# Performance work log

Hardware: AMD Instinct MI355X
Metric: run time of the kernel (lower is better)

## Reference

```python
import jax, jax.numpy as jnp
import numpy as np
from jax import lax

B, Q, C, K = 256, 900, 91, 300  # batch, queries, classes, topk boxes for eval
SIGMA = 0.5                      # gaussian decay variance
SCORE_THR = 1e-3                 # hardcoded score_threshold in soft_nms


def setup_inputs() -> dict:
    key = jax.random.key(0)
    k1, k2, k3 = jax.random.split(key, 3)
    pred_logits = jax.random.normal(k1, (B, Q, C), dtype=jnp.float32)
    pred_boxes = jax.random.uniform(k2, (B, Q, 4), dtype=jnp.float32)  # cxcywh in [0,1]
    target_sizes = jax.random.randint(k3, (B, 2), 480, 1334).astype(jnp.float32)  # (h, w)
    return {"pred_logits": pred_logits, "pred_boxes": pred_boxes, "target_sizes": target_sizes}


def _iou_one(box, boxes):
    # box: [4] xyxy, boxes: [K,4] xyxy -> iou: [K]
    area1 = (box[2] - box[0]) * (box[3] - box[1])
    area2 = (boxes[:, 2] - boxes[:, 0]) * (boxes[:, 3] - boxes[:, 1])
    lt = jnp.maximum(box[:2], boxes[:, :2])
    rb = jnp.minimum(box[2:], boxes[:, 2:])
    wh = jnp.clip(rb - lt, 0.0)
    inter = wh[:, 0] * wh[:, 1]
    return inter / (area1 + area2 - inter)


def _soft_nms(boxes, scores):
    # boxes: [K,4], scores: [K]. Sequential gaussian soft-NMS, faithful to source
    # (source's iou_threshold arg is unused; decay applied to all trailing boxes).
    idxs = jnp.arange(K)

    def step(carry, i):
        bxs, scs, active = carry
        m = jnp.argmax(jnp.where(idxs >= i, scs, -jnp.inf))
        cond = active & (scs[m] >= SCORE_THR)  # break condition (sticky)
        # swap rows i <-> m
        bi, bm = bxs[i], bxs[m]
        si, sm = scs[i], scs[m]
        b2 = bxs.at[i].set(bm).at[m].set(bi)
        s2 = scs.at[i].set(sm).at[m].set(si)
        # gaussian decay on boxes after i
        decay = jnp.exp(-(_iou_one(b2[i], b2) ** 2) / SIGMA)
        s2 = s2 * jnp.where(idxs > i, decay, 1.0)
        return (jnp.where(cond, b2, bxs), jnp.where(cond, s2, scs), cond), None

    (boxes, scores, _), _ = lax.scan(step, (boxes, scores, jnp.array(True)), idxs)
    keep = scores > SCORE_THR
    return boxes, scores, keep


def _postprocess(pred_logits, pred_boxes, target_sizes):
    prob = jax.nn.sigmoid(pred_logits)                       # [B,Q,C]
    flat = prob.reshape(B, Q * C)
    topk_values, topk_indexes = lax.top_k(flat, K)           # [B,K]
    scores = topk_values
    topk_boxes = topk_indexes // C                           # query index
    labels = topk_indexes % C                                # class index
    # cxcywh -> xyxy
    cx, cy, w, h = jnp.split(pred_boxes, 4, axis=-1)
    xyxy = jnp.concatenate([cx - 0.5 * w, cy - 0.5 * h, cx + 0.5 * w, cy + 0.5 * h], axis=-1)
    gidx = jnp.broadcast_to(topk_boxes[..., None], (B, K, 4))
    boxes = jnp.take_along_axis(xyxy, gidx, axis=1)          # [B,K,4]
    img_h, img_w = target_sizes[:, 0], target_sizes[:, 1]
    scale = jnp.stack([img_w, img_h, img_w, img_h], axis=1)[:, None, :]
    boxes = boxes * scale
    boxes, scores, keep = jax.vmap(_soft_nms)(boxes, scores)
    return scores, labels, boxes, keep


def reference(pred_logits, pred_boxes, target_sizes):
    # Returns dense arrays + keep mask (ragged filtering expressed as a boolean mask
    # to stay jit-compatible). labels are intentionally NOT reordered by soft-NMS
    # swaps, matching the source's in-place mutation semantics.
    return _postprocess(pred_logits, pred_boxes, target_sizes)
```

## Files before the change

kernel.cpp:

```cpp
#include <hip/hip_runtime.h>
#include <cfloat>
#include <cmath>

#pragma clang fp contract(off)

#define BB 256
#define QQ 900
#define CC 91
#define KK 300
#define QC 81900
#define MAXIDX 81899
#define NF4 20475
#define STRIPC 30
#define SKCAP 512

#define OFF_SCORES 0
#define OFF_LABELS 76800
#define OFF_BOXES  153600
#define OFF_KEEP   460800

__device__ __forceinline__ unsigned int wave_max_u32(unsigned int x) {
#define DPP_MAX(ctrl, rmask)                                                   \
  { unsigned int tmp = (unsigned int)__builtin_amdgcn_update_dpp(              \
        (int)x, (int)x, ctrl, rmask, 0xF, false);                              \
    x = tmp > x ? tmp : x; }
  DPP_MAX(0x111, 0xF)
  DPP_MAX(0x112, 0xF)
  DPP_MAX(0x114, 0xF)
  DPP_MAX(0x118, 0xF)
  DPP_MAX(0x142, 0xA)
  DPP_MAX(0x143, 0xC)
#undef DPP_MAX
  return (unsigned int)__builtin_amdgcn_readlane((int)x, 63);
}

__device__ __forceinline__ float rdlane_f(float x, int l) {
  return __uint_as_float(
      (unsigned int)__builtin_amdgcn_readlane((int)__float_as_uint(x), l));
}

__device__ __forceinline__ float soft_decay(float s, float4 bb, float4 bm,
                                            float area1) {
  float area2 = (bb.z - bb.x) * (bb.w - bb.y);
  float ltx = fmaxf(bm.x, bb.x);
  float lty = fmaxf(bm.y, bb.y);
  float rbx = fminf(bm.z, bb.z);
  float rby = fminf(bm.w, bb.w);
  float whx = fmaxf(rbx - ltx, 0.0f);
  float why = fmaxf(rby - lty, 0.0f);
  float inter = whx * why;
  float iou = inter / ((area1 + area2) - inter);
  return s * expf(-(iou * iou) * 2.0f);
}

__global__ __launch_bounds__(256, 1) void fused_kernel(
    const float* __restrict__ logits,
    const float* __restrict__ boxes_in,
    const float* __restrict__ tsizes,
    float* __restrict__ out)
{
  const int b = blockIdx.x;
  const int t = threadIdx.x;
  const int lane = t & 63;
  const int w = t >> 6;

  __shared__ unsigned int strip[STRIPC + 1][256];
  __shared__ int hist[2048];
  __shared__ int suffix[256];
  __shared__ unsigned long long skey[SKCAP];
  __shared__ float  sc_lds[KK];
  __shared__ float4 bx_lds[KK];
  __shared__ unsigned long long wkey[2][4];
  __shared__ float4 wbox[2][4];
  __shared__ float  isc_s[2];
  __shared__ float4 ibx_s[2];
  __shared__ int cnt2, cstar_s, cutbin;

  if (t == 0) { cnt2 = 0; cstar_s = 0; cutbin = 0; }
  for (int i = t; i < 2048; i += 256) hist[i] = 0;
  __syncthreads();

  const float4* row = (const float4*)(logits + (size_t)b * QC);
  unsigned int nh = 0;

  float4 f[8];
#define PROC_ELEM(xv, idxv)                                                    \
  {                                                                            \
    bool hit = (xv) > 2.0f;                                                    \
    unsigned int pos = hit ? nh : (unsigned int)STRIPC;                        \
    strip[pos][t] = (unsigned int)(idxv);                                      \
    nh = hit ? nh + 1u : nh;                                                   \
    nh = nh > (unsigned int)STRIPC ? (unsigned int)STRIPC : nh;                \
  }

  for (int k0 = 0; k0 + 8 <= 79; k0 += 8) {
#pragma unroll
    for (int u = 0; u < 8; ++u) f[u] = row[t + (k0 + u) * 256];
#pragma unroll
    for (int u = 0; u < 8; ++u) {
      const int i4 = (t + (k0 + u) * 256) * 4;
      PROC_ELEM(f[u].x, i4 + 0)
      PROC_ELEM(f[u].y, i4 + 1)
      PROC_ELEM(f[u].z, i4 + 2)
      PROC_ELEM(f[u].w, i4 + 3)
    }
  }
  for (int k = 72; k < 79; ++k) {
    float4 x4 = row[t + k * 256];
    const int i4 = (t + k * 256) * 4;
    PROC_ELEM(x4.x, i4 + 0)
    PROC_ELEM(x4.y, i4 + 1)
    PROC_ELEM(x4.z, i4 + 2)
    PROC_ELEM(x4.w, i4 + 3)
  }
  if (t < NF4 - 79 * 256) {
    float4 x4 = row[t + 79 * 256];
    const int i4 = (t + 79 * 256) * 4;
    PROC_ELEM(x4.x, i4 + 0)
    PROC_ELEM(x4.y, i4 + 1)
    PROC_ELEM(x4.z, i4 + 2)
    PROC_ELEM(x4.w, i4 + 3)
  }
#undef PROC_ELEM

  const float* lrow = logits + (size_t)b * QC;
  for (unsigned int j = 0; j < nh; ++j) {
    unsigned int idx = strip[j][t];
    float x = lrow[idx];
    unsigned int bin = (__float_as_uint(x) - 0x40000000u) >> 13;
    bin = bin > 2047u ? 2047u : bin;
    atomicAdd(&hist[bin], 1);
  }
  __syncthreads();

  {
    int cs = 0;
#pragma unroll
    for (int k = 0; k < 8; ++k) cs += hist[t * 8 + k];
    suffix[t] = cs;
  }
  __syncthreads();
  for (int off = 1; off < 256; off <<= 1) {
    int add = (t + off < 256) ? suffix[t + off] : 0;
    __syncthreads();
    suffix[t] += add;
    __syncthreads();
  }
  if (suffix[t] >= KK && (t == 255 || suffix[t + 1] < KK)) cstar_s = t;
  __syncthreads();
  if (t == 0) {
    int cs = cstar_s;
    int acc = (cs < 255) ? suffix[cs + 1] : 0;
    for (int k = 7; k >= 0; --k) {
      acc += hist[cs * 8 + k];
      if (acc >= KK) { cutbin = cs * 8 + k; break; }
    }
  }
  __syncthreads();
  const int cb = cutbin;

  for (unsigned int j = 0; j < nh; ++j) {
    unsigned int idx = strip[j][t];
    float x = lrow[idx];
    unsigned int bin = (__float_as_uint(x) - 0x40000000u) >> 13;
    bin = bin > 2047u ? 2047u : bin;
    if ((int)bin >= cb) {
      float sgm = 1.0f / (1.0f + expf(-x));
      int p = atomicAdd(&cnt2, 1);
      if (p < SKCAP)
        skey[p] = ((unsigned long long)__float_as_uint(sgm) << 17) |
                  (unsigned long long)(MAXIDX - idx);
    }
  }
  __syncthreads();
  const int M = min(cnt2, SKCAP);

  const float img_h = tsizes[b * 2 + 0];
  const float img_w = tsizes[b * 2 + 1];
  for (int o = t; o < M; o += 256) {
    unsigned long long ko = skey[o];
    int r = 0;
    for (int k = 0; k < M; ++k) r += (skey[k] > ko) ? 1 : 0;
    if (r < KK) {
      unsigned int bits = (unsigned int)(ko >> 17);
      int idx = MAXIDX - (int)(ko & 0x1FFFFull);
      int q   = idx / CC;
      int lab = idx - q * CC;

      out[OFF_LABELS + b * KK + r] = (float)lab;
      sc_lds[r] = __uint_as_float(bits);

      float4 bxv = ((const float4*)boxes_in)[(size_t)b * QQ + q];
      float cx = bxv.x, cy = bxv.y, ww = bxv.z, hh = bxv.w;
      float4 bo;
      bo.x = (cx - 0.5f * ww) * img_w;
      bo.y = (cy - 0.5f * hh) * img_h;
      bo.z = (cx + 0.5f * ww) * img_w;
      bo.w = (cy + 0.5f * hh) * img_h;
      bx_lds[r] = bo;
    }
  }
  __syncthreads();

  const int e1 = t;
  const bool v2 = (lane < 11);
  const int e2 = 256 + w * 11 + lane;

  float  sc1 = sc_lds[e1];
  float4 bx1 = bx_lds[e1];
  float  sc2 = 0.0f;
  float4 bx2 = make_float4(0.f, 0.f, 0.f, 0.f);
  if (v2) { sc2 = sc_lds[e2]; bx2 = bx_lds[e2]; }

  for (int i = 0; i < KK; ++i) {
    const int p = i & 1;

    bool a1 = (e1 >= i);
    bool a2 = v2 && (e2 >= i);
    unsigned int u1 = a1 ? __float_as_uint(sc1) : 0u;
    unsigned int u2 = a2 ? __float_as_uint(sc2) : 0u;
    unsigned int um = u1 > u2 ? u1 : u2;
    unsigned int wm = wave_max_u32(um);
    unsigned long long m1 = __ballot(a1 && u1 == wm);
    unsigned long long m2 = __ballot(a2 && u2 == wm);
    int lstar;
    bool prim;
    if (m1) { lstar = __ffsll((long long)m1) - 1; prim = true; }
    else    { lstar = m2 ? __ffsll((long long)m2) - 1 : 0; prim = false; }
    int estar = prim ? (w * 64 + lstar) : (256 + w * 11 + lstar);
    float cbx, cby, cbz, cbw;
    if (prim) {
      cbx = rdlane_f(bx1.x, lstar); cby = rdlane_f(bx1.y, lstar);
      cbz = rdlane_f(bx1.z, lstar); cbw = rdlane_f(bx1.w, lstar);
    } else {
      cbx = rdlane_f(bx2.x, lstar); cby = rdlane_f(bx2.y, lstar);
      cbz = rdlane_f(bx2.z, lstar); cbw = rdlane_f(bx2.w, lstar);
    }
    if (lane == 0) {
      wkey[p][w] = ((unsigned long long)wm << 32) |
                   (unsigned long long)(511 - estar);
      wbox[p][w] = make_float4(cbx, cby, cbz, cbw);
    }
    if (e1 == i)        { isc_s[p] = sc1; ibx_s[p] = bx1; }
    if (v2 && e2 == i)  { isc_s[p] = sc2; ibx_s[p] = bx2; }
    __syncthreads();

    unsigned long long k0 = wkey[p][0], k1 = wkey[p][1], k2 = wkey[p][2],
                       k3 = wkey[p][3];
    float4 wb0 = wbox[p][0], wb1 = wbox[p][1], wb2 = wbox[p][2],
           wb3 = wbox[p][3];
    float  si = isc_s[p];
    float4 bi = ibx_s[p];

    unsigned long long best = k0;
    best = k1 > best ? k1 : best;
    best = k2 > best ? k2 : best;
    best = k3 > best ? k3 : best;
    float sm = __uint_as_float((unsigned int)(best >> 32));
    if (!(sm >= 0.001f)) break;
    int mi = 511 - (int)(best & 0x1FFull);
    int widx = (mi < 256) ? (mi >> 6) : ((mi - 256) / 11);
    float4 bm = wb0;
    if (widx == 1) bm = wb1;
    if (widx == 2) bm = wb2;
    if (widx == 3) bm = wb3;

    if (e1 == i)  { sc1 = sm; bx1 = bm; }
    if (e1 == mi) { sc1 = si; bx1 = bi; }
    if (v2) {
      if (e2 == i)  { sc2 = sm; bx2 = bm; }
      if (e2 == mi) { sc2 = si; bx2 = bi; }
    }

    float area1 = (bm.z - bm.x) * (bm.w - bm.y);
    if (e1 > i)       sc1 = soft_decay(sc1, bx1, bm, area1);
    if (v2 && e2 > i) sc2 = soft_decay(sc2, bx2, bm, area1);
  }

  out[OFF_SCORES + b * KK + e1] = sc1;
  ((float4*)(out + OFF_BOXES))[b * KK + e1] = bx1;
  out[OFF_KEEP + b * KK + e1] = (sc1 > 0.001f) ? 1.0f : 0.0f;
  if (v2) {
    out[OFF_SCORES + b * KK + e2] = sc2;
    ((float4*)(out + OFF_BOXES))[b * KK + e2] = bx2;
    out[OFF_KEEP + b * KK + e2] = (sc2 > 0.001f) ? 1.0f : 0.0f;
  }
}

extern "C" void kernel_launch(void* const* d_in, const int* in_sizes, int n_in,
                              void* d_out, int out_size, void* d_ws, size_t ws_size,
                              hipStream_t stream) {
  const float* pred_logits = (const float*)d_in[0];
  const float* pred_boxes  = (const float*)d_in[1];
  const float* tsizes      = (const float*)d_in[2];
  float* out = (float*)d_out;
  (void)d_ws; (void)ws_size;

  fused_kernel<<<BB, 256, 0, stream>>>(pred_logits, pred_boxes, tsizes, out);
}
```

Before: 349.2 us.

## Run soft-NMS loop in a single wavefront to drop per-iteration block barriers

The sequential soft-NMS loop moves from all four waves, which synchronised through LDS and __syncthreads every iteration, to wave 0 alone. Each lane holds five elements in registers, and the argmax, swap and decay use DPP reductions, ballots and readlane only. Box areas are cached per element so they are not recomputed each step. This removes 300 block barriers and LDS round trips per image, at the cost of each lane doing about five times more decay math per step, with the outer loop over the five register slots fully unrolled.

```diff
diff --git a/kernel.cpp b/kernel.cpp
--- a/kernel.cpp
+++ b/kernel.cpp
@@ -39,20 +39,6 @@
       (unsigned int)__builtin_amdgcn_readlane((int)__float_as_uint(x), l));
 }
 
-__device__ __forceinline__ float soft_decay(float s, float4 bb, float4 bm,
-                                            float area1) {
-  float area2 = (bb.z - bb.x) * (bb.w - bb.y);
-  float ltx = fmaxf(bm.x, bb.x);
-  float lty = fmaxf(bm.y, bb.y);
-  float rbx = fminf(bm.z, bb.z);
-  float rby = fminf(bm.w, bb.w);
-  float whx = fmaxf(rbx - ltx, 0.0f);
-  float why = fmaxf(rby - lty, 0.0f);
-  float inter = whx * why;
-  float iou = inter / ((area1 + area2) - inter);
-  return s * expf(-(iou * iou) * 2.0f);
-}
-
 __global__ __launch_bounds__(256, 1) void fused_kernel(
     const float* __restrict__ logits,
     const float* __restrict__ boxes_in,
@@ -70,10 +56,6 @@
   __shared__ unsigned long long skey[SKCAP];
   __shared__ float  sc_lds[KK];
   __shared__ float4 bx_lds[KK];
-  __shared__ unsigned long long wkey[2][4];
-  __shared__ float4 wbox[2][4];
-  __shared__ float  isc_s[2];
-  __shared__ float4 ibx_s[2];
   __shared__ int cnt2, cstar_s, cutbin;
 
   if (t == 0) { cnt2 = 0; cstar_s = 0; cutbin = 0; }
@@ -202,88 +184,99 @@
   }
   __syncthreads();
 
-  const int e1 = t;
-  const bool v2 = (lane < 11);
-  const int e2 = 256 + w * 11 + lane;
-
-  float  sc1 = sc_lds[e1];
-  float4 bx1 = bx_lds[e1];
-  float  sc2 = 0.0f;
-  float4 bx2 = make_float4(0.f, 0.f, 0.f, 0.f);
-  if (v2) { sc2 = sc_lds[e2]; bx2 = bx_lds[e2]; }
-
-  for (int i = 0; i < KK; ++i) {
-    const int p = i & 1;
-
-    bool a1 = (e1 >= i);
-    bool a2 = v2 && (e2 >= i);
-    unsigned int u1 = a1 ? __float_as_uint(sc1) : 0u;
-    unsigned int u2 = a2 ? __float_as_uint(sc2) : 0u;
-    unsigned int um = u1 > u2 ? u1 : u2;
-    unsigned int wm = wave_max_u32(um);
-    unsigned long long m1 = __ballot(a1 && u1 == wm);
-    unsigned long long m2 = __ballot(a2 && u2 == wm);
-    int lstar;
-    bool prim;
-    if (m1) { lstar = __ffsll((long long)m1) - 1; prim = true; }
-    else    { lstar = m2 ? __ffsll((long long)m2) - 1 : 0; prim = false; }
-    int estar = prim ? (w * 64 + lstar) : (256 + w * 11 + lstar);
-    float cbx, cby, cbz, cbw;
-    if (prim) {
-      cbx = rdlane_f(bx1.x, lstar); cby = rdlane_f(bx1.y, lstar);
-      cbz = rdlane_f(bx1.z, lstar); cbw = rdlane_f(bx1.w, lstar);
-    } else {
-      cbx = rdlane_f(bx2.x, lstar); cby = rdlane_f(bx2.y, lstar);
-      cbz = rdlane_f(bx2.z, lstar); cbw = rdlane_f(bx2.w, lstar);
-    }
-    if (lane == 0) {
-      wkey[p][w] = ((unsigned long long)wm << 32) |
-                   (unsigned long long)(511 - estar);
-      wbox[p][w] = make_float4(cbx, cby, cbz, cbw);
-    }
-    if (e1 == i)        { isc_s[p] = sc1; ibx_s[p] = bx1; }
-    if (v2 && e2 == i)  { isc_s[p] = sc2; ibx_s[p] = bx2; }
-    __syncthreads();
-
-    unsigned long long k0 = wkey[p][0], k1 = wkey[p][1], k2 = wkey[p][2],
-                       k3 = wkey[p][3];
-    float4 wb0 = wbox[p][0], wb1 = wbox[p][1], wb2 = wbox[p][2],
-           wb3 = wbox[p][3];
-    float  si = isc_s[p];
-    float4 bi = ibx_s[p];
-
-    unsigned long long best = k0;
-    best = k1 > best ? k1 : best;
-    best = k2 > best ? k2 : best;
-    best = k3 > best ? k3 : best;
-    float sm = __uint_as_float((unsigned int)(best >> 32));
-    if (!(sm >= 0.001f)) break;
-    int mi = 511 - (int)(best & 0x1FFull);
-    int widx = (mi < 256) ? (mi >> 6) : ((mi - 256) / 11);
-    float4 bm = wb0;
-    if (widx == 1) bm = wb1;
-    if (widx == 2) bm = wb2;
-    if (widx == 3) bm = wb3;
-
-    if (e1 == i)  { sc1 = sm; bx1 = bm; }
-    if (e1 == mi) { sc1 = si; bx1 = bi; }
-    if (v2) {
-      if (e2 == i)  { sc2 = sm; bx2 = bm; }
-      if (e2 == mi) { sc2 = si; bx2 = bi; }
-    }
-
-    float area1 = (bm.z - bm.x) * (bm.w - bm.y);
-    if (e1 > i)       sc1 = soft_decay(sc1, bx1, bm, area1);
-    if (v2 && e2 > i) sc2 = soft_decay(sc2, bx2, bm, area1);
-  }
-
-  out[OFF_SCORES + b * KK + e1] = sc1;
-  ((float4*)(out + OFF_BOXES))[b * KK + e1] = bx1;
-  out[OFF_KEEP + b * KK + e1] = (sc1 > 0.001f) ? 1.0f : 0.0f;
-  if (v2) {
-    out[OFF_SCORES + b * KK + e2] = sc2;
-    ((float4*)(out + OFF_BOXES))[b * KK + e2] = bx2;
-    out[OFF_KEEP + b * KK + e2] = (sc2 > 0.001f) ? 1.0f : 0.0f;
+  if (w == 0) {
+    float  sc[5];
+    float4 bxr[5];
+    float  a2[5];
+#pragma unroll
+    for (int j = 0; j < 5; ++j) {
+      int e = j * 64 + lane;
+      if (e < KK) { sc[j] = sc_lds[e]; bxr[j] = bx_lds[e]; }
+      else        { sc[j] = 0.0f; bxr[j] = make_float4(0.f, 0.f, 0.f, 0.f); }
+      a2[j] = (bxr[j].z - bxr[j].x) * (bxr[j].w - bxr[j].y);
+    }
+
+#pragma unroll
+    for (int ji = 0; ji < 5; ++ji) {
+      const int iiend = (ji == 4) ? 44 : 64;
+#pragma unroll 1
+      for (int ii = 0; ii < iiend; ++ii) {
+        const int i = ji * 64 + ii;
+
+        unsigned int lm = (lane >= ii) ? __float_as_uint(sc[ji]) : 0u;
+#pragma unroll
+        for (int jj = ji + 1; jj < 5; ++jj) {
+          unsigned int v = __float_as_uint(sc[jj]);
+          lm = v > lm ? v : lm;
+        }
+        const unsigned int wm = wave_max_u32(lm);
+        const float sm = __uint_as_float(wm);
+        if (!(sm >= 0.001f)) goto nms_done;
+
+        int jstar = ji, lstar = 0;
+        float4 bm;
+        {
+          bool found = false;
+#pragma unroll
+          for (int jj = ji; jj < 5; ++jj) {
+            if (!found) {
+              bool cand = (__float_as_uint(sc[jj]) == wm);
+              if (jj == ji) cand = cand && (lane >= ii);
+              unsigned long long mm = __ballot(cand);
+              if (mm) {
+                jstar = jj;
+                lstar = __ffsll((long long)mm) - 1;
+                bm.x = rdlane_f(bxr[jj].x, lstar);
+                bm.y = rdlane_f(bxr[jj].y, lstar);
+                bm.z = rdlane_f(bxr[jj].z, lstar);
+                bm.w = rdlane_f(bxr[jj].w, lstar);
+                found = true;
+              }
+            }
+          }
+        }
+
+        const float si = rdlane_f(sc[ji], ii);
+        const float ai = rdlane_f(a2[ji], ii);
+        float4 bi;
+        bi.x = rdlane_f(bxr[ji].x, ii);
+        bi.y = rdlane_f(bxr[ji].y, ii);
+        bi.z = rdlane_f(bxr[ji].z, ii);
+        bi.w = rdlane_f(bxr[ji].w, ii);
+        const float area1 = (bm.z - bm.x) * (bm.w - bm.y);
+
+        if (lane == ii) { sc[ji] = sm; bxr[ji] = bm; a2[ji] = area1; }
+#pragma unroll
+        for (int jj = ji; jj < 5; ++jj)
+          if (jj == jstar && lane == lstar) { sc[jj] = si; bxr[jj] = bi; a2[jj] = ai; }
+
+#pragma unroll
+        for (int jj = ji; jj < 5; ++jj) {
+          const bool act = (jj > ji) || (lane > ii);
+          float4 bb = bxr[jj];
+          float ltx = fmaxf(bm.x, bb.x);
+          float lty = fmaxf(bm.y, bb.y);
+          float rbx = fminf(bm.z, bb.z);
+          float rby = fminf(bm.w, bb.w);
+          float whx = fmaxf(rbx - ltx, 0.0f);
+          float why = fmaxf(rby - lty, 0.0f);
+          float inter = whx * why;
+          float iou = inter / ((area1 + a2[jj]) - inter);
+          float d = expf(-(iou * iou) * 2.0f);
+          sc[jj] = act ? sc[jj] * d : sc[jj];
+        }
+      }
+    }
+nms_done:
+#pragma unroll
+    for (int j = 0; j < 5; ++j) {
+      int e = j * 64 + lane;
+      if (e < KK) {
+        out[OFF_SCORES + b * KK + e] = sc[j];
+        ((float4*)(out + OFF_BOXES))[b * KK + e] = bxr[j];
+        out[OFF_KEEP + b * KK + e] = (sc[j] > 0.001f) ? 1.0f : 0.0f;
+      }
+    }
   }
 }
 
```

Result: faster. 298.6 us (-14.5%).
